# Kernel tuning notes

Hardware: AMD Instinct MI355X
Metric: run time of the kernel (lower is better)

The kernel has to match this reference:

```python
import jax, jax.numpy as jnp
import numpy as np

EPS = 1e-12
SAMPLE_SIZES = (100, 50)  # hardcoded in the torch module


def setup_inputs() -> dict:
    key = jax.random.key(0)
    k1, k2, k3, k4 = jax.random.split(key, 4)
    N, E, C_IN, C_HID, C_OUT = 50000, 1600000, 256, 64, 128
    x = jax.random.normal(k1, (N, C_IN), dtype=jnp.float32)
    edge_index = jax.random.randint(k2, (2, E), 0, N, dtype=jnp.int64)
    W1 = jax.random.normal(k3, (C_IN, C_HID), dtype=jnp.float32) / np.sqrt(C_IN)
    b1 = jnp.zeros((C_HID,), dtype=jnp.float32)
    W2 = jax.random.normal(k4, (C_HID, C_OUT), dtype=jnp.float32) / np.sqrt(C_HID)
    b2 = jnp.zeros((C_OUT,), dtype=jnp.float32)
    return {"x": x, "edge_index": edge_index, "W1": W1, "b1": b1, "W2": W2, "b2": b2}


def _sample_mask(edge_index, num_samples, key):
    """Keep at most num_samples random out-edges per source node (fixed-shape mask)."""
    src = edge_index[0]
    E = src.shape[0]
    pri = jax.random.uniform(key, (E,))
    order = jnp.lexsort((pri, src))            # group by src, random order within group
    src_sorted = src[order]
    first = jnp.searchsorted(src_sorted, src_sorted, side="left")
    rank = jnp.arange(E) - first               # rank within each src group
    keep_sorted = rank < num_samples
    mask = jnp.zeros((E,), dtype=jnp.float32).at[order].set(keep_sorted.astype(jnp.float32))
    return mask


def _gcn_conv(x, edge_index, edge_weight, W, b, num_nodes):
    """PyG GCNConv: self-loops + symmetric deg^-1/2 normalization, aggregate at dst."""
    h = x @ W                                   # [N, out]
    src, dst = edge_index[0], edge_index[1]
    loop = jnp.arange(num_nodes, dtype=src.dtype)
    src_f = jnp.concatenate([src, loop])
    dst_f = jnp.concatenate([dst, loop])
    w_f = jnp.concatenate([edge_weight, jnp.ones((num_nodes,), dtype=edge_weight.dtype)])
    deg = jax.ops.segment_sum(w_f, dst_f, num_segments=num_nodes)
    dinv = jnp.where(deg > 0, jax.lax.rsqrt(jnp.maximum(deg, EPS)), 0.0)
    norm = w_f * dinv[src_f] * dinv[dst_f]      # [E+N]
    msgs = h[src_f] * norm[:, None]             # gather + scale (memory bound)
    out = jax.ops.segment_sum(msgs, dst_f, num_segments=num_nodes)
    return out + b


def reference(x, edge_index, W1, b1, W2, b2):
    num_nodes = x.shape[0]
    skey = jax.random.key(42)
    sk1, sk2 = jax.random.split(skey)
    m1 = _sample_mask(edge_index, SAMPLE_SIZES[0], sk1)
    m2 = _sample_mask(edge_index, SAMPLE_SIZES[1], sk2)
    h = _gcn_conv(x, edge_index, m1, W1, b1, num_nodes)
    h = jax.nn.relu(h)
    h = h / jnp.maximum(jnp.linalg.norm(h, axis=-1, keepdims=True), EPS)  # F.normalize(p=2)
    out = _gcn_conv(h, edge_index, m2, W2, b2, num_nodes)
    return out
```

## Files before the change

### kernel.cpp

```cpp
#include <hip/hip_runtime.h>

typedef unsigned int u32;
typedef unsigned short u16;
typedef unsigned long long u64;
typedef __attribute__((ext_vector_type(8))) short bh8;
typedef __attribute__((ext_vector_type(4))) float f4;

#define HMAX 1024
#define MAXD 128
#define SB_CAP 24576
#define DB_CAP 6144
#define SBCHUNK 2048
#define SPLIT 8
#define G1S 72
#define DROP_CAP 32768

__device__ inline f4 mfma16(bh8 a, bh8 b, f4 c) {
  return __builtin_amdgcn_mfma_f32_16x16x32_bf16(a, b, c, 0, 0, 0);
}

__host__ __device__ inline void tf2x32(u32 k0, u32 k1, u32 x0, u32 x1, u32& o0, u32& o1) {
  u32 ks2 = k0 ^ k1 ^ 0x1BD11BDAu;
#define ROTL32(x,d) (((x)<<(d))|((x)>>(32-(d))))
#define TFR(r) { x0 += x1; x1 = ROTL32(x1,(r)); x1 ^= x0; }
  x0 += k0; x1 += k1;
  TFR(13) TFR(15) TFR(26) TFR(6)
  x0 += k1; x1 += ks2 + 1u;
  TFR(17) TFR(29) TFR(16) TFR(24)
  x0 += ks2; x1 += k0 + 2u;
  TFR(13) TFR(15) TFR(26) TFR(6)
  x0 += k0; x1 += k1 + 3u;
  TFR(17) TFR(29) TFR(16) TFR(24)
  x0 += k1; x1 += ks2 + 4u;
  TFR(13) TFR(15) TFR(26) TFR(6)
  x0 += ks2; x1 += k0 + 5u;
  o0 = x0; o1 = x1;
#undef TFR
#undef ROTL32
}

__device__ inline u16 f2bf(float f) {
  u32 u = __float_as_uint(f);
  return (u16)((u + 0x7FFFu + ((u >> 16) & 1u)) >> 16);
}
__device__ inline float bflo(u32 u) { return __uint_as_float(u << 16); }
__device__ inline float bfhi(u32 u) { return __uint_as_float(u & 0xFFFF0000u); }

struct BinS { u32 lsrc[128]; u32 lbase[128]; u32 ldst[512]; u32 dbase[512]; };
struct GemS { u16 xs[64 * G1S]; u16 ws[64 * G1S]; };

__global__ __launch_bounds__(256) void k_mega1(const int* __restrict__ ei, int E,
                                               const float* __restrict__ x, int N,
                                               const float* __restrict__ W1, const float* __restrict__ W2,
                                               int* __restrict__ srcCnt, u32* __restrict__ srcRec,
                                               int* __restrict__ dstCnt, u64* __restrict__ dstRec,
                                               u16* __restrict__ h1b, u16* __restrict__ W2t, int nBin) {
  __shared__ __align__(16) char smem[sizeof(GemS)];
  int t = threadIdx.x;
  int bid = blockIdx.x;
  int nGemm = (N + 63) >> 6;

  if (bid < nBin) {
    BinS& S = *(BinS*)smem;
    if (t < 128) S.lsrc[t] = 0;
    for (int v = t; v < 512; v += 256) S.ldst[v] = 0;
    __syncthreads();
    int lo = bid * SBCHUNK;
    int hi = min(lo + SBCHUNK, E);
    int e0 = lo + 8 * t;
    int nv = min(8, hi - e0); if (nv < 0) nv = 0;
    int sv[8], dv[8];
    if (nv == 8 && ((E & 3) == 0)) {
      int4 a0 = *((const int4*)(ei + e0));
      int4 a1 = *((const int4*)(ei + e0 + 4));
      int4 b0 = *((const int4*)(ei + E + e0));
      int4 b1 = *((const int4*)(ei + E + e0 + 4));
      sv[0]=a0.x; sv[1]=a0.y; sv[2]=a0.z; sv[3]=a0.w; sv[4]=a1.x; sv[5]=a1.y; sv[6]=a1.z; sv[7]=a1.w;
      dv[0]=b0.x; dv[1]=b0.y; dv[2]=b0.z; dv[3]=b0.w; dv[4]=b1.x; dv[5]=b1.y; dv[6]=b1.z; dv[7]=b1.w;
    } else {
      for (int j = 0; j < nv; ++j) { sv[j] = ei[e0 + j]; dv[j] = ei[E + e0 + j]; }
    }
    for (int j = 0; j < nv; ++j) {
      atomicAdd(&S.lsrc[sv[j] >> 9], 1u);
      atomicAdd(&S.ldst[dv[j] >> 7], 1u);
    }
    __syncthreads();
    if (t < 128) {
      u32 c = S.lsrc[t];
      if (c) S.lbase[t] = (u32)atomicAdd(&srcCnt[t], (int)c);
      S.lsrc[t] = 0;
    }
    for (int v = t; v < 512; v += 256) {
      u32 cd = S.ldst[v];
      if (cd) S.dbase[v] = (u32)atomicAdd(&dstCnt[v], (int)cd);
      S.ldst[v] = 0;
    }
    __syncthreads();
    for (int j = 0; j < nv; ++j) {
      int s = sv[j], d = dv[j];
      u32 i = (u32)(e0 + j);
      int bs = s >> 9;
      u32 slot = S.lbase[bs] + atomicAdd(&S.lsrc[bs], 1u);
      if (slot < SB_CAP) srcRec[(size_t)bs * SB_CAP + slot] = ((u32)(s & 511) << 21) | i;
      int bd = d >> 7;
      u32 slot2 = S.dbase[bd] + atomicAdd(&S.ldst[bd], 1u);
      if (slot2 < DB_CAP)
        dstRec[(size_t)bd * DB_CAP + slot2] = ((u64)(d & 127) << 37) | ((u64)(u32)s << 21) | i;
    }
  } else if (bid < nBin + nGemm) {
    GemS& G = *(GemS*)smem;
    int wv = t >> 6, lane = t & 63;
    int qd = lane >> 4, md = lane & 15;
    int m0 = (bid - nBin) * 64;
    if (m0 >= N) return;
    f4 acc[4] = {};
    for (int ks = 0; ks < 256; ks += 64) {
      __syncthreads();
#pragma unroll
      for (int i = 0; i < 4; ++i) {
        int f = t + 256 * i;
        int r = f >> 4, c4 = f & 15;
        int grow = m0 + r; if (grow >= N) grow = N - 1;
        float4 v = ((const float4*)x)[(size_t)grow * 64 + (ks >> 2) + c4];
        u32 p0 = (u32)f2bf(v.x) | ((u32)f2bf(v.y) << 16);
        u32 p1 = (u32)f2bf(v.z) | ((u32)f2bf(v.w) << 16);
        *((uint2*)(G.xs + r * G1S + c4 * 4)) = make_uint2(p0, p1);
      }
#pragma unroll
      for (int i = 0; i < 4; ++i) {
        int f = t + 256 * i;
        int k = f >> 4, c4 = f & 15;
        float4 v = ((const float4*)W1)[(ks + k) * 16 + c4];
        int n0 = c4 * 4;
        G.ws[(n0 + 0) * G1S + k] = f2bf(v.x);
        G.ws[(n0 + 1) * G1S + k] = f2bf(v.y);
        G.ws[(n0 + 2) * G1S + k] = f2bf(v.z);
        G.ws[(n0 + 3) * G1S + k] = f2bf(v.w);
      }
      __syncthreads();
#pragma unroll
      for (int kk = 0; kk < 64; kk += 32) {
        bh8 af = *((const bh8*)(G.xs + (16 * wv + md) * G1S + kk + qd * 8));
#pragma unroll
        for (int nt = 0; nt < 4; ++nt) {
          bh8 bf = *((const bh8*)(G.ws + (nt * 16 + md) * G1S + kk + qd * 8));
          acc[nt] = mfma16(af, bf, acc[nt]);
        }
      }
    }
#pragma unroll
    for (int nt = 0; nt < 4; ++nt)
#pragma unroll
      for (int r = 0; r < 4; ++r) {
        int row = m0 + 16 * wv + qd * 4 + r;
        if (row < N) h1b[(size_t)row * 64 + nt * 16 + md] = f2bf(acc[nt][r]);
      }
  } else {
    for (int e = t; e < 64 * 128; e += 256) {
      int n = e & 127, k = e >> 7;
      W2t[n * 64 + k] = f2bf(W2[k * 128 + n]);
    }
  }
}

__global__ __launch_bounds__(256) void k_shist(const int* __restrict__ srcCnt, const u32* __restrict__ srcRec,
                                               int* __restrict__ outdegB) {
  int bk = blockIdx.x >> 3;
  int part = blockIdx.x & (SPLIT - 1);
  int total = min(srcCnt[bk], SB_CAP);
  int lo = total * part / SPLIT;
  int hi = total * (part + 1) / SPLIT;
  __shared__ u32 cnt[512];
  int t = threadIdx.x;
  cnt[t] = 0; cnt[t + 256] = 0;
  __syncthreads();
  const u32* R = srcRec + (size_t)bk * SB_CAP;
  for (int i = lo + t; i < hi; i += 256) atomicAdd(&cnt[R[i] >> 21], 1u);
  __syncthreads();
  int base = bk * 512;
  for (int v = t; v < 512; v += 256) {
    u32 c = cnt[v];
    if (c) atomicAdd(&outdegB[base + v], (int)c);
  }
}

__global__ __launch_bounds__(256) void k_hdetect(const int* __restrict__ outdegB, u32* __restrict__ idAB,
                                                 int* __restrict__ hcA, int* __restrict__ hcB,
                                                 const int* __restrict__ dstCnt, int* __restrict__ bucketBase,
                                                 int* __restrict__ dptr, int nbD, int N) {
  if (blockIdx.x == 0 && threadIdx.x == 0) {
    int s = 0;
    for (int i = 0; i < nbD; ++i) { bucketBase[i] = s; s += min(dstCnt[i], DB_CAP); }
    bucketBase[nbD] = s;
    dptr[N] = s;
  }
  int v = blockIdx.x * 256 + threadIdx.x;
  if (v >= N) return;
  int dg = outdegB[v];
  u32 pk = 0;
  if (dg > 50) {
    int idb = atomicAdd(hcB, 1);
    if (idb < HMAX) pk = (u32)(idb + 1);
    if (dg > 100) {
      int ida = atomicAdd(hcA, 1);
      if (ida < HMAX) pk |= (u32)(ida + 1) << 16;
    }
  }
  idAB[v] = pk;
}

__global__ __launch_bounds__(256) void k_hfill(const int* __restrict__ srcCnt, const u32* __restrict__ srcRec,
                                               const u32* __restrict__ idAB,
                                               int* __restrict__ bcA, u64* __restrict__ bukA,
                                               int* __restrict__ bcB, u64* __restrict__ bukB,
                                               u32 kaA, u32 kbA, u32 kaB, u32 kbB) {
  int bk = blockIdx.x >> 3;
  int part = blockIdx.x & (SPLIT - 1);
  int total = min(srcCnt[bk], SB_CAP);
  int lo = total * part / SPLIT;
  int hi = total * (part + 1) / SPLIT;
  const u32* R = srcRec + (size_t)bk * SB_CAP;
  int base = bk * 512;
  for (int i = lo + threadIdx.x; i < hi; i += 256) {
    u32 r = R[i];
    u32 pk = idAB[base + (int)(r >> 21)];
    if (pk) {
      u32 e = r & 0x1FFFFFu;
      int idb = (int)(pk & 0xFFFFu) - 1;
      if (idb >= 0) {
        u32 w0, w1; tf2x32(kaB, kbB, 0u, e, w0, w1);
        int slot = atomicAdd(&bcB[idb], 1);
        if (slot < MAXD) bukB[(size_t)idb * MAXD + slot] = ((u64)((w0 ^ w1) >> 9) << 32) | e;
      }
      int ida = (int)(pk >> 16) - 1;
      if (ida >= 0) {
        u32 w0, w1; tf2x32(kaA, kbA, 0u, e, w0, w1);
        int slot = atomicAdd(&bcA[ida], 1);
        if (slot < MAXD) bukA[(size_t)ida * MAXD + slot] = ((u64)((w0 ^ w1) >> 9) << 32) | e;
      }
    }
  }
}

__global__ __launch_bounds__(256) void k_rank2(const int* __restrict__ hcA, const int* __restrict__ bcA,
                                               const u64* __restrict__ bukA,
                                               const int* __restrict__ hcB, const int* __restrict__ bcB,
                                               const u64* __restrict__ bukB,
                                               int* __restrict__ dropCnt, u32* __restrict__ dropList) {
  bool isA = blockIdx.x < (HMAX / 4);
  int bx = isA ? blockIdx.x : blockIdx.x - HMAX / 4;
  const int* hcount = isA ? hcA : hcB;
  const int* bcount = isA ? bcA : bcB;
  const u64* bucket = isA ? bukA : bukB;
  int S = isA ? 100 : 50;
  u32 bit = isA ? 1u : 2u;
  int wid = (bx * 256 + (int)threadIdx.x) >> 6;
  int lane = threadIdx.x & 63;
  int hc = hcount[0]; if (hc > HMAX) hc = HMAX;
  if (wid >= hc) return;
  int d = bcount[wid]; if (d > MAXD) d = MAXD;
  const u64* B = bucket + (size_t)wid * MAXD;
  for (int i = lane; i < d; i += 64) {
    u64 ki = B[i];
    int rank = 0;
    for (int j = 0; j < d; ++j) rank += (B[j] < ki) ? 1 : 0;
    if (rank >= S) {
      int idx = atomicAdd(dropCnt, 1);
      if (idx < DROP_CAP) dropList[idx] = ((u32)ki & 0x1FFFFFu) | (bit << 21);
    }
  }
}

__global__ __launch_bounds__(256) void k_phase2(const int* __restrict__ bucketBase,
                                                const int* __restrict__ dstCnt,
                                                const u64* __restrict__ dstRec,
                                                const int* __restrict__ dropCnt,
                                                const u32* __restrict__ dropList,
                                                u32* __restrict__ entries, int* __restrict__ dptr,
                                                float* __restrict__ dinv1, float* __restrict__ dinv2, int N) {
  int b = blockIdx.x;
  int base = bucketBase[b];
  int cnt0 = min(dstCnt[b], DB_CAP);
  const u64* R = dstRec + (size_t)b * DB_CAP;
  __shared__ u32 cnt[128];
  __shared__ u32 htab[4096];
  __shared__ u32 ws2[2];
  int t = threadIdx.x;
  if (t < 128) cnt[t] = 0;
  for (int i = t; i < 4096; i += 256) htab[i] = 0xFFFFFFFFu;
  __syncthreads();
  int dc = min(dropCnt[0], 3072);
  for (int i = t; i < dc; i += 256) {
    u32 pk = dropList[i];
    u32 key = pk & 0x1FFFFFu;
    u32 h = (key * 2654435761u) >> 20;
    while (true) {
      u32 old = atomicCAS(&htab[h], 0xFFFFFFFFu, pk);
      if (old == 0xFFFFFFFFu) break;
      if ((old & 0x1FFFFFu) == key) { atomicOr(&htab[h], pk & 0x00600000u); break; }
      h = (h + 1) & 4095;
    }
  }
  __syncthreads();
  for (int i = t; i < cnt0; i += 256) {
    u64 r = R[i];
    u32 dl = (u32)(r >> 37) & 127u;
    u32 key = (u32)r & 0x1FFFFFu;
    u32 drop = 0;
    u32 h = (key * 2654435761u) >> 20;
    while (true) {
      u32 v = htab[h];
      if (v == 0xFFFFFFFFu) break;
      if ((v & 0x1FFFFFu) == key) { drop = (v >> 21) & 3u; break; }
      h = (h + 1) & 4095;
    }
    u32 add = 1u + ((1u - (drop & 1u)) << 10) + ((1u - ((drop >> 1) & 1u)) << 20);
    atomicAdd(&cnt[dl], add);
  }
  __syncthreads();
  u32 c0 = (t < 128) ? cnt[t] : 0;
  u32 tot = c0 & 1023u;
  int lane = t & 63, w = t >> 6;
  u32 incl = tot;
  for (int off = 1; off < 64; off <<= 1) {
    u32 nbv = (u32)__shfl_up((int)incl, off, 64);
    if (lane >= off) incl += nbv;
  }
  if (lane == 63 && w == 0) ws2[0] = incl;
  __syncthreads();
  u32 excl = incl - tot + ((w == 1) ? ws2[0] : 0u);
  int v0 = b * 128 + t;
  if (t < 128 && v0 < N) {
    dptr[v0] = base + (int)excl;
    dinv1[v0] = 1.0f / sqrtf((float)(((c0 >> 10) & 1023u) + 1u));
    dinv2[v0] = 1.0f / sqrtf((float)(((c0 >> 20) & 1023u) + 1u));
  }
  __syncthreads();
  if (t < 128) cnt[t] = excl;
  __syncthreads();
  for (int i = t; i < cnt0; i += 256) {
    u64 r = R[i];
    u32 dl = (u32)(r >> 37) & 127u;
    u32 key = (u32)r & 0x1FFFFFu;
    u32 drop = 0;
    u32 h = (key * 2654435761u) >> 20;
    while (true) {
      u32 v = htab[h];
      if (v == 0xFFFFFFFFu) break;
      if ((v & 0x1FFFFFu) == key) { drop = (v >> 21) & 3u; break; }
      h = (h + 1) & 4095;
    }
    u32 src = (u32)(r >> 21) & 0xFFFFu;
    u32 slot = atomicAdd(&cnt[dl], 1u);
    entries[base + slot] = src | ((drop & 1u) ? 0u : (1u << 30)) | ((drop & 2u) ? 0u : (1u << 31));
  }
}

__global__ __launch_bounds__(256) void k_conv1n(const int* __restrict__ ptr, const u32* __restrict__ entries,
                                                const float* __restrict__ dinv1, const uint4* __restrict__ h1q,
                                                const float* __restrict__ b1, uint4* __restrict__ hnbq, int N) {
  int wid = (blockIdx.x * 256 + threadIdx.x) >> 6;
  if (wid >= N) return;
  int lane = threadIdx.x & 63;
  int lo8 = lane & 7, grp = lane >> 3;
  int beg = ptr[wid], end = ptr[wid + 1];
  float a0 = 0.f, a1 = 0.f, a2 = 0.f, a3 = 0.f, a4 = 0.f, a5 = 0.f, a6 = 0.f, a7 = 0.f;
  for (int cb = beg; cb < end; cb += 64) {
    int idx = cb + lane;
    float wgt = 0.f; int s = 0;
    if (idx < end) {
      u32 e = entries[idx];
      s = (int)(e & 0xFFFFu);
      if (e & (1u << 30)) wgt = dinv1[s];
    }
    int nq = (min(64, end - cb) + 7) >> 3;
    int j = grp;
    float w = __shfl(wgt, j, 64);
    int sj = __shfl(s, j, 64);
    uint4 uv = h1q[(size_t)sj * 8 + lo8];
    for (int i = 1; i < nq; ++i) {
      int j2 = j + 8;
      float w2 = __shfl(wgt, j2, 64);
      int s2 = __shfl(s, j2, 64);
      uint4 uv2 = h1q[(size_t)s2 * 8 + lo8];
      a0 = fmaf(w, bflo(uv.x), a0); a1 = fmaf(w, bfhi(uv.x), a1);
      a2 = fmaf(w, bflo(uv.y), a2); a3 = fmaf(w, bfhi(uv.y), a3);
      a4 = fmaf(w, bflo(uv.z), a4); a5 = fmaf(w, bfhi(uv.z), a5);
      a6 = fmaf(w, bflo(uv.w), a6); a7 = fmaf(w, bfhi(uv.w), a7);
      w = w2; uv = uv2; j = j2;
    }
    a0 = fmaf(w, bflo(uv.x), a0); a1 = fmaf(w, bfhi(uv.x), a1);
    a2 = fmaf(w, bflo(uv.y), a2); a3 = fmaf(w, bfhi(uv.y), a3);
    a4 = fmaf(w, bflo(uv.z), a4); a5 = fmaf(w, bfhi(uv.z), a5);
    a6 = fmaf(w, bflo(uv.w), a6); a7 = fmaf(w, bfhi(uv.w), a7);
  }
#pragma unroll
  for (int off = 8; off < 64; off <<= 1) {
    a0 += __shfl_xor(a0, off, 64); a1 += __shfl_xor(a1, off, 64);
    a2 += __shfl_xor(a2, off, 64); a3 += __shfl_xor(a3, off, 64);
    a4 += __shfl_xor(a4, off, 64); a5 += __shfl_xor(a5, off, 64);
    a6 += __shfl_xor(a6, off, 64); a7 += __shfl_xor(a7, off, 64);
  }
  float dv = dinv1[wid];
  uint4 uo = h1q[(size_t)wid * 8 + lo8];
  a0 = fmaf(dv, bflo(uo.x), a0); a1 = fmaf(dv, bfhi(uo.x), a1);
  a2 = fmaf(dv, bflo(uo.y), a2); a3 = fmaf(dv, bfhi(uo.y), a3);
  a4 = fmaf(dv, bflo(uo.z), a4); a5 = fmaf(dv, bfhi(uo.z), a5);
  a6 = fmaf(dv, bflo(uo.w), a6); a7 = fmaf(dv, bfhi(uo.w), a7);
  float4 bbA = ((const float4*)b1)[lo8 * 2];
  float4 bbB = ((const float4*)b1)[lo8 * 2 + 1];
  float o0 = fmaxf(fmaf(dv, a0, bbA.x), 0.f);
  float o1 = fmaxf(fmaf(dv, a1, bbA.y), 0.f);
  float o2 = fmaxf(fmaf(dv, a2, bbA.z), 0.f);
  float o3 = fmaxf(fmaf(dv, a3, bbA.w), 0.f);
  float o4 = fmaxf(fmaf(dv, a4, bbB.x), 0.f);
  float o5 = fmaxf(fmaf(dv, a5, bbB.y), 0.f);
  float o6 = fmaxf(fmaf(dv, a6, bbB.z), 0.f);
  float o7 = fmaxf(fmaf(dv, a7, bbB.w), 0.f);
  float ss = fmaf(o0, o0, fmaf(o1, o1, fmaf(o2, o2, o3 * o3)))
           + fmaf(o4, o4, fmaf(o5, o5, fmaf(o6, o6, o7 * o7)));
#pragma unroll
  for (int off = 1; off < 8; off <<= 1) ss += __shfl_xor(ss, off, 8);
  float sc = 1.f / fmaxf(sqrtf(ss), 1e-12f);
  if (lane < 8) {
    uint4 pv;
    pv.x = (u32)f2bf(o0 * sc) | ((u32)f2bf(o1 * sc) << 16);
    pv.y = (u32)f2bf(o2 * sc) | ((u32)f2bf(o3 * sc) << 16);
    pv.z = (u32)f2bf(o4 * sc) | ((u32)f2bf(o5 * sc) << 16);
    pv.w = (u32)f2bf(o6 * sc) | ((u32)f2bf(o7 * sc) << 16);
    hnbq[(size_t)wid * 8 + lo8] = pv;
  }
}

__global__ __launch_bounds__(256) void k_agg2(const int* __restrict__ ptr, const u32* __restrict__ entries,
                                              const float* __restrict__ dinv2, const uint4* __restrict__ hnq,
                                              uint4* __restrict__ agg2q, int N) {
  int wid = (blockIdx.x * 256 + threadIdx.x) >> 6;
  if (wid >= N) return;
  int lane = threadIdx.x & 63;
  int lo8 = lane & 7, grp = lane >> 3;
  int beg = ptr[wid], end = ptr[wid + 1];
  float a0 = 0.f, a1 = 0.f, a2 = 0.f, a3 = 0.f, a4 = 0.f, a5 = 0.f, a6 = 0.f, a7 = 0.f;
  for (int cb = beg; cb < end; cb += 64) {
    int idx = cb + lane;
    float wgt = 0.f; int s = 0;
    if (idx < end) {
      u32 e = entries[idx];
      s = (int)(e & 0xFFFFu);
      if (e & (1u << 31)) wgt = dinv2[s];
    }
    int nq = (min(64, end - cb) + 7) >> 3;
    int j = grp;
    float w = __shfl(wgt, j, 64);
    int sj = __shfl(s, j, 64);
    uint4 uv = hnq[(size_t)sj * 8 + lo8];
    for (int i = 1; i < nq; ++i) {
      int j2 = j + 8;
      float w2 = __shfl(wgt, j2, 64);
      int s2 = __shfl(s, j2, 64);
      uint4 uv2 = hnq[(size_t)s2 * 8 + lo8];
      a0 = fmaf(w, bflo(uv.x), a0); a1 = fmaf(w, bfhi(uv.x), a1);
      a2 = fmaf(w, bflo(uv.y), a2); a3 = fmaf(w, bfhi(uv.y), a3);
      a4 = fmaf(w, bflo(uv.z), a4); a5 = fmaf(w, bfhi(uv.z), a5);
      a6 = fmaf(w, bflo(uv.w), a6); a7 = fmaf(w, bfhi(uv.w), a7);
      w = w2; uv = uv2; j = j2;
    }
    a0 = fmaf(w, bflo(uv.x), a0); a1 = fmaf(w, bfhi(uv.x), a1);
    a2 = fmaf(w, bflo(uv.y), a2); a3 = fmaf(w, bfhi(uv.y), a3);
    a4 = fmaf(w, bflo(uv.z), a4); a5 = fmaf(w, bfhi(uv.z), a5);
    a6 = fmaf(w, bflo(uv.w), a6); a7 = fmaf(w, bfhi(uv.w), a7);
  }
#pragma unroll
  for (int off = 8; off < 64; off <<= 1) {
    a0 += __shfl_xor(a0, off, 64); a1 += __shfl_xor(a1, off, 64);
    a2 += __shfl_xor(a2, off, 64); a3 += __shfl_xor(a3, off, 64);
    a4 += __shfl_xor(a4, off, 64); a5 += __shfl_xor(a5, off, 64);
    a6 += __shfl_xor(a6, off, 64); a7 += __shfl_xor(a7, off, 64);
  }
  float dv = dinv2[wid];
  uint4 uo = hnq[(size_t)wid * 8 + lo8];
  a0 = fmaf(dv, bflo(uo.x), a0); a1 = fmaf(dv, bfhi(uo.x), a1);
  a2 = fmaf(dv, bflo(uo.y), a2); a3 = fmaf(dv, bfhi(uo.y), a3);
  a4 = fmaf(dv, bflo(uo.z), a4); a5 = fmaf(dv, bfhi(uo.z), a5);
  a6 = fmaf(dv, bflo(uo.w), a6); a7 = fmaf(dv, bfhi(uo.w), a7);
  if (lane < 8) {
    uint4 pv;
    pv.x = (u32)f2bf(dv * a0) | ((u32)f2bf(dv * a1) << 16);
    pv.y = (u32)f2bf(dv * a2) | ((u32)f2bf(dv * a3) << 16);
    pv.z = (u32)f2bf(dv * a4) | ((u32)f2bf(dv * a5) << 16);
    pv.w = (u32)f2bf(dv * a6) | ((u32)f2bf(dv * a7) << 16);
    agg2q[(size_t)wid * 8 + lo8] = pv;
  }
}

#define G2S 72
__global__ __launch_bounds__(256) void k_gemm2f(const u16* __restrict__ aggb, const u16* __restrict__ W2t,
                                                const float* __restrict__ b2, float* __restrict__ out, int N) {
  __shared__ u16 hs[64 * G2S];
  __shared__ u16 ws[128 * G2S];
  int t = threadIdx.x;
  int wv = t >> 6, lane = t & 63;
  int qd = lane >> 4, md = lane & 15;
  int m0 = blockIdx.x * 64;
#pragma unroll
  for (int i = 0; i < 2; ++i) {
    int cc = t + 256 * i;
    int r = cc >> 3, kc = (cc & 7) * 8;
    int grow = m0 + r; if (grow >= N) grow = N - 1;
    *((uint4*)(hs + r * G2S + kc)) = *((const uint4*)(aggb + (size_t)grow * 64 + kc));
  }
#pragma unroll
  for (int i = 0; i < 4; ++i) {
    int cc = t + 256 * i;
    int n = cc >> 3, kc = (cc & 7) * 8;
    *((uint4*)(ws + n * G2S + kc)) = *((const uint4*)(W2t + n * 64 + kc));
  }
  __syncthreads();
  f4 acc[8] = {};
#pragma unroll
  for (int kk = 0; kk < 64; kk += 32) {
    bh8 af = *((const bh8*)(hs + (16 * wv + md) * G2S + kk + qd * 8));
#pragma unroll
    for (int nt = 0; nt < 8; ++nt) {
      bh8 bf = *((const bh8*)(ws + (nt * 16 + md) * G2S + kk + qd * 8));
      acc[nt] = mfma16(af, bf, acc[nt]);
    }
  }
#pragma unroll
  for (int nt = 0; nt < 8; ++nt) {
    float bv = b2[nt * 16 + md];
#pragma unroll
    for (int r = 0; r < 4; ++r) {
      int row = m0 + 16 * wv + qd * 4 + r;
      if (row < N) out[(size_t)row * 128 + nt * 16 + md] = acc[nt][r] + bv;
    }
  }
}

extern "C" void kernel_launch(void* const* d_in, const int* in_sizes, int n_in,
                              void* d_out, int out_size, void* d_ws, size_t ws_size,
                              hipStream_t stream) {
  const float* x  = (const float*)d_in[0];
  const int*   ei = (const int*)d_in[1];
  const float* W1 = (const float*)d_in[2];
  const float* b1 = (const float*)d_in[3];
  const float* W2 = (const float*)d_in[4];
  const float* b2 = (const float*)d_in[5];
  const int N = in_sizes[0] / 256;
  const int E = in_sizes[1] / 2;
  const int nbS = (N + 511) >> 9;
  const int nbD = (N + 127) >> 7;

  u32 sk1a, sk1b, sk2a, sk2b;
  tf2x32(0u, 42u, 0u, 0u, sk1a, sk1b);
  tf2x32(0u, 42u, 0u, 1u, sk2a, sk2b);

  char* p = (char*)d_ws;
  auto alloc = [&](size_t bytes) { char* r = p; p += (bytes + 255) & ~(size_t)255; return r; };
  int* dstCnt      = (int*)alloc(512 * 4);
  int* srcCnt      = (int*)alloc(128 * 4);
  int* hcbA        = (int*)alloc((size_t)(1 + HMAX) * 4);
  int* hcbB        = (int*)alloc((size_t)(1 + HMAX) * 4);
  int* outdegB     = (int*)alloc((size_t)nbS * 512 * 4);
  int* dropCnt     = (int*)alloc(256);
  char* zero_end = p;
  u32* dropList = (u32*)alloc((size_t)DROP_CAP * 4);
  u32* idAB     = (u32*)alloc((size_t)nbS * 512 * 4);
  u16* h1b      = (u16*)alloc((size_t)N * 64 * 2);
  u16* hnb      = (u16*)alloc((size_t)N * 64 * 2);
  u16* agg2b    = (u16*)alloc((size_t)N * 64 * 2);
  float* dinv1  = (float*)alloc((size_t)N * 4);
  float* dinv2  = (float*)alloc((size_t)N * 4);
  int* dptr     = (int*)alloc((size_t)(N + 1) * 4);
  int* bucketBase = (int*)alloc(513 * 4);
  u32* entries  = (u32*)alloc((size_t)E * 4);
  u32* srcRec   = (u32*)alloc((size_t)nbS * SB_CAP * 4);
  u64* dstRec   = (u64*)alloc((size_t)nbD * DB_CAP * 8);
  u64* bukA     = (u64*)alloc((size_t)HMAX * MAXD * 8);
  u64* bukB     = (u64*)alloc((size_t)HMAX * MAXD * 8);
  u16* W2t      = (u16*)alloc(64 * 128 * 2);

  int* hcA = hcbA; int* bcA = hcbA + 1;
  int* hcB = hcbB; int* bcB = hcbB + 1;

  hipMemsetAsync(dstCnt, 0x00, (size_t)(zero_end - (char*)dstCnt), stream);

  const int nBin = (E + SBCHUNK - 1) / SBCHUNK;
  const int nGemm = (N + 63) / 64;
  k_mega1<<<nBin + nGemm + 1, 256, 0, stream>>>(ei, E, x, N, W1, W2,
                                                srcCnt, srcRec, dstCnt, dstRec, h1b, W2t, nBin);
  k_shist<<<nbS * SPLIT, 256, 0, stream>>>(srcCnt, srcRec, outdegB);
  k_hdetect<<<(N + 255) / 256, 256, 0, stream>>>(outdegB, idAB, hcA, hcB, dstCnt, bucketBase,
                                                 dptr, nbD, N);
  k_hfill<<<nbS * SPLIT, 256, 0, stream>>>(srcCnt, srcRec, idAB, bcA, bukA, bcB, bukB,
                                           sk1a, sk1b, sk2a, sk2b);
  k_rank2<<<HMAX / 2, 256, 0, stream>>>(hcA, bcA, bukA, hcB, bcB, bukB, dropCnt, dropList);
  k_phase2<<<nbD, 256, 0, stream>>>(bucketBase, dstCnt, dstRec, dropCnt, dropList,
                                    entries, dptr, dinv1, dinv2, N);
  k_conv1n<<<(N * 64 + 255) / 256, 256, 0, stream>>>(dptr, entries, dinv1, (const uint4*)h1b, b1,
                                                     (uint4*)hnb, N);
  k_agg2<<<(N * 64 + 255) / 256, 256, 0, stream>>>(dptr, entries, dinv2, (const uint4*)hnb,
                                                   (uint4*)agg2b, N);
  k_gemm2f<<<(N + 63) / 64, 256, 0, stream>>>(agg2b, W2t, b2, (float*)d_out, N);
}
```

Baseline: 301.3 us.

## Enlarge binning chunks, pad global bucket counters, parallelize bucket prefix scan

Each binning block now handles 8192 edges in four 2048-edge sub-passes instead of 2048, reading the edges twice. This cuts the number of blocks issuing global atomics on the bucket counters. The counters are spaced 16 ints apart so each sits on its own cache line, reducing atomic contention. The serial single-thread prefix sum over the destination bucket counts becomes a shared-memory parallel scan in block 0. The costs are an extra edge read, less block-level parallelism in the binning phase, and a larger counter area, which is still zeroed because it lies before zero_end.

```diff
diff --git a/kernel.cpp b/kernel.cpp
--- a/kernel.cpp
+++ b/kernel.cpp
@@ -10,10 +10,11 @@
 #define MAXD 128
 #define SB_CAP 24576
 #define DB_CAP 6144
-#define SBCHUNK 2048
+#define SBCHUNK 8192
 #define SPLIT 8
 #define G1S 72
 #define DROP_CAP 32768
+#define CPAD 16
 
 __device__ inline f4 mfma16(bh8 a, bh8 b, f4 c) {
   return __builtin_amdgcn_mfma_f32_16x16x32_bf16(a, b, c, 0, 0, 0);
@@ -67,45 +68,59 @@
     __syncthreads();
     int lo = bid * SBCHUNK;
     int hi = min(lo + SBCHUNK, E);
-    int e0 = lo + 8 * t;
-    int nv = min(8, hi - e0); if (nv < 0) nv = 0;
-    int sv[8], dv[8];
-    if (nv == 8 && ((E & 3) == 0)) {
-      int4 a0 = *((const int4*)(ei + e0));
-      int4 a1 = *((const int4*)(ei + e0 + 4));
-      int4 b0 = *((const int4*)(ei + E + e0));
-      int4 b1 = *((const int4*)(ei + E + e0 + 4));
-      sv[0]=a0.x; sv[1]=a0.y; sv[2]=a0.z; sv[3]=a0.w; sv[4]=a1.x; sv[5]=a1.y; sv[6]=a1.z; sv[7]=a1.w;
-      dv[0]=b0.x; dv[1]=b0.y; dv[2]=b0.z; dv[3]=b0.w; dv[4]=b1.x; dv[5]=b1.y; dv[6]=b1.z; dv[7]=b1.w;
-    } else {
-      for (int j = 0; j < nv; ++j) { sv[j] = ei[e0 + j]; dv[j] = ei[E + e0 + j]; }
-    }
-    for (int j = 0; j < nv; ++j) {
-      atomicAdd(&S.lsrc[sv[j] >> 9], 1u);
-      atomicAdd(&S.ldst[dv[j] >> 7], 1u);
+    bool fast = ((E & 3) == 0);
+
+    auto loadE = [&](int e0, int nv, int* sv, int* dv) {
+      if (nv == 8 && fast) {
+        int4 a0 = *((const int4*)(ei + e0));
+        int4 a1 = *((const int4*)(ei + e0 + 4));
+        int4 b0 = *((const int4*)(ei + E + e0));
+        int4 b1 = *((const int4*)(ei + E + e0 + 4));
+        sv[0]=a0.x; sv[1]=a0.y; sv[2]=a0.z; sv[3]=a0.w; sv[4]=a1.x; sv[5]=a1.y; sv[6]=a1.z; sv[7]=a1.w;
+        dv[0]=b0.x; dv[1]=b0.y; dv[2]=b0.z; dv[3]=b0.w; dv[4]=b1.x; dv[5]=b1.y; dv[6]=b1.z; dv[7]=b1.w;
+      } else {
+        for (int j = 0; j < nv; ++j) { sv[j] = ei[e0 + j]; dv[j] = ei[E + e0 + j]; }
+      }
+    };
+
+    for (int sub = 0; sub < SBCHUNK; sub += 2048) {
+      int e0 = lo + sub + 8 * t;
+      int nv = min(8, hi - e0); if (nv < 0) nv = 0;
+      int sv[8], dv[8];
+      loadE(e0, nv, sv, dv);
+      for (int j = 0; j < nv; ++j) {
+        atomicAdd(&S.lsrc[sv[j] >> 9], 1u);
+        atomicAdd(&S.ldst[dv[j] >> 7], 1u);
+      }
     }
     __syncthreads();
     if (t < 128) {
       u32 c = S.lsrc[t];
-      if (c) S.lbase[t] = (u32)atomicAdd(&srcCnt[t], (int)c);
+      if (c) S.lbase[t] = (u32)atomicAdd(&srcCnt[t * CPAD], (int)c);
       S.lsrc[t] = 0;
     }
     for (int v = t; v < 512; v += 256) {
       u32 cd = S.ldst[v];
-      if (cd) S.dbase[v] = (u32)atomicAdd(&dstCnt[v], (int)cd);
+      if (cd) S.dbase[v] = (u32)atomicAdd(&dstCnt[v * CPAD], (int)cd);
       S.ldst[v] = 0;
     }
     __syncthreads();
-    for (int j = 0; j < nv; ++j) {
-      int s = sv[j], d = dv[j];
-      u32 i = (u32)(e0 + j);
-      int bs = s >> 9;
-      u32 slot = S.lbase[bs] + atomicAdd(&S.lsrc[bs], 1u);
-      if (slot < SB_CAP) srcRec[(size_t)bs * SB_CAP + slot] = ((u32)(s & 511) << 21) | i;
-      int bd = d >> 7;
-      u32 slot2 = S.dbase[bd] + atomicAdd(&S.ldst[bd], 1u);
-      if (slot2 < DB_CAP)
-        dstRec[(size_t)bd * DB_CAP + slot2] = ((u64)(d & 127) << 37) | ((u64)(u32)s << 21) | i;
+    for (int sub = 0; sub < SBCHUNK; sub += 2048) {
+      int e0 = lo + sub + 8 * t;
+      int nv = min(8, hi - e0); if (nv < 0) nv = 0;
+      int sv[8], dv[8];
+      loadE(e0, nv, sv, dv);
+      for (int j = 0; j < nv; ++j) {
+        int s = sv[j], d = dv[j];
+        u32 i = (u32)(e0 + j);
+        int bs = s >> 9;
+        u32 slot = S.lbase[bs] + atomicAdd(&S.lsrc[bs], 1u);
+        if (slot < SB_CAP) srcRec[(size_t)bs * SB_CAP + slot] = ((u32)(s & 511) << 21) | i;
+        int bd = d >> 7;
+        u32 slot2 = S.dbase[bd] + atomicAdd(&S.ldst[bd], 1u);
+        if (slot2 < DB_CAP)
+          dstRec[(size_t)bd * DB_CAP + slot2] = ((u64)(d & 127) << 37) | ((u64)(u32)s << 21) | i;
+      }
     }
   } else if (bid < nBin + nGemm) {
     GemS& G = *(GemS*)smem;
@@ -167,7 +182,7 @@
                                                int* __restrict__ outdegB) {
   int bk = blockIdx.x >> 3;
   int part = blockIdx.x & (SPLIT - 1);
-  int total = min(srcCnt[bk], SB_CAP);
+  int total = min(srcCnt[bk * CPAD], SB_CAP);
   int lo = total * part / SPLIT;
   int hi = total * (part + 1) / SPLIT;
   __shared__ u32 cnt[512];
@@ -188,13 +203,27 @@
                                                  int* __restrict__ hcA, int* __restrict__ hcB,
                                                  const int* __restrict__ dstCnt, int* __restrict__ bucketBase,
                                                  int* __restrict__ dptr, int nbD, int N) {
-  if (blockIdx.x == 0 && threadIdx.x == 0) {
-    int s = 0;
-    for (int i = 0; i < nbD; ++i) { bucketBase[i] = s; s += min(dstCnt[i], DB_CAP); }
-    bucketBase[nbD] = s;
-    dptr[N] = s;
-  }
-  int v = blockIdx.x * 256 + threadIdx.x;
+  int t = threadIdx.x;
+  if (blockIdx.x == 0) {
+    __shared__ int sc[512], tp[512];
+    for (int i = t; i < 512; i += 256) sc[i] = (i < nbD) ? min(dstCnt[i * CPAD], DB_CAP) : 0;
+    __syncthreads();
+    for (int off = 1; off < 512; off <<= 1) {
+      for (int i = t; i < 512; i += 256) tp[i] = sc[i] + ((i >= off) ? sc[i - off] : 0);
+      __syncthreads();
+      for (int i = t; i < 512; i += 256) sc[i] = tp[i];
+      __syncthreads();
+    }
+    for (int i = t; i < 512; i += 256) {
+      if (i < nbD) bucketBase[i] = (i == 0) ? 0 : sc[i - 1];
+    }
+    if (t == 0) {
+      int tot = sc[nbD - 1];
+      bucketBase[nbD] = tot;
+      dptr[N] = tot;
+    }
+  }
+  int v = blockIdx.x * 256 + t;
   if (v >= N) return;
   int dg = outdegB[v];
   u32 pk = 0;
@@ -216,7 +245,7 @@
                                                u32 kaA, u32 kbA, u32 kaB, u32 kbB) {
   int bk = blockIdx.x >> 3;
   int part = blockIdx.x & (SPLIT - 1);
-  int total = min(srcCnt[bk], SB_CAP);
+  int total = min(srcCnt[bk * CPAD], SB_CAP);
   int lo = total * part / SPLIT;
   int hi = total * (part + 1) / SPLIT;
   const u32* R = srcRec + (size_t)bk * SB_CAP;
@@ -280,7 +309,7 @@
                                                 float* __restrict__ dinv1, float* __restrict__ dinv2, int N) {
   int b = blockIdx.x;
   int base = bucketBase[b];
-  int cnt0 = min(dstCnt[b], DB_CAP);
+  int cnt0 = min(dstCnt[b * CPAD], DB_CAP);
   const u64* R = dstRec + (size_t)b * DB_CAP;
   __shared__ u32 cnt[128];
   __shared__ u32 htab[4096];
@@ -557,8 +586,8 @@
 
   char* p = (char*)d_ws;
   auto alloc = [&](size_t bytes) { char* r = p; p += (bytes + 255) & ~(size_t)255; return r; };
-  int* dstCnt      = (int*)alloc(512 * 4);
-  int* srcCnt      = (int*)alloc(128 * 4);
+  int* dstCnt      = (int*)alloc((size_t)512 * CPAD * 4);
+  int* srcCnt      = (int*)alloc((size_t)128 * CPAD * 4);
   int* hcbA        = (int*)alloc((size_t)(1 + HMAX) * 4);
   int* hcbB        = (int*)alloc((size_t)(1 + HMAX) * 4);
   int* outdegB     = (int*)alloc((size_t)nbS * 512 * 4);
```

New measurement: 264.1 us. 12.3% less time.
